# Kernel optimization log

Measured on AMD Instinct MI355X. Metric: run time of the kernel, lower is better.

The kernel has to match this reference:

```python
import jax, jax.numpy as jnp
import numpy as np

N = 50000      # nodes
E = 800000     # edges (before self-loops)
IN_DIM = 128
HID = 64
HEADS = 4
NEG_SLOPE = 0.2  # PyG GATConv default leaky-relu slope


def setup_inputs() -> dict:
    key = jax.random.key(0)
    ks = jax.random.split(key, 12)
    s = 0.05
    return {
        "x": jax.random.normal(ks[0], (N, IN_DIM), jnp.float32),
        "edge_index": jax.random.randint(ks[1], (2, E), 0, N, dtype=jnp.int64),
        "W1": jax.random.normal(ks[2], (IN_DIM, HEADS * HID), jnp.float32) * s,
        "att1_src": jax.random.normal(ks[3], (HEADS, HID), jnp.float32) * s,
        "att1_dst": jax.random.normal(ks[4], (HEADS, HID), jnp.float32) * s,
        "b1": jax.random.normal(ks[5], (HEADS * HID,), jnp.float32) * s,
        "W2": jax.random.normal(ks[6], (HEADS * HID, HID), jnp.float32) * s,
        "att2_src": jax.random.normal(ks[7], (1, HID), jnp.float32) * s,
        "att2_dst": jax.random.normal(ks[8], (1, HID), jnp.float32) * s,
        "b2": jax.random.normal(ks[9], (HID,), jnp.float32) * s,
        "Wc": jax.random.normal(ks[10], (HID, 2), jnp.float32) * s,
        "bc": jax.random.normal(ks[11], (2,), jnp.float32) * s,
    }


def _gat_conv(x, src, dst, W, a_src, a_dst, b, heads, d, concat):
    """PyG GATConv (eval mode): gather-score-segment_softmax-scatter."""
    n = x.shape[0]
    h = (x @ W).reshape(n, heads, d)               # [N,H,D]
    alpha_s = jnp.einsum('nhd,hd->nh', h, a_src)   # [N,H]
    alpha_d = jnp.einsum('nhd,hd->nh', h, a_dst)
    e = jax.nn.leaky_relu(alpha_s[src] + alpha_d[dst], NEG_SLOPE)  # [E,H]
    # softmax over incoming edges of each destination node
    m = jax.ops.segment_max(e, dst, num_segments=n)                # [N,H]
    ex = jnp.exp(e - m[dst])
    den = jax.ops.segment_sum(ex, dst, num_segments=n)
    alpha = ex / den[dst]                                          # [E,H]
    out = jax.ops.segment_sum(h[src] * alpha[:, :, None], dst, num_segments=n)  # [N,H,D]
    out = out.reshape(n, heads * d) if concat else out.mean(axis=1)
    return out + b


def reference(x, edge_index, W1, att1_src, att1_dst, b1,
              W2, att2_src, att2_dst, b2, Wc, bc):
    n = x.shape[0]
    # PyG GATConv adds self-loops by default
    loops = jnp.arange(n, dtype=edge_index.dtype)
    src = jnp.concatenate([edge_index[0], loops])
    dst = jnp.concatenate([edge_index[1], loops])
    h1 = jax.nn.elu(_gat_conv(x, src, dst, W1, att1_src, att1_dst, b1, HEADS, HID, True))
    h2 = jax.nn.elu(_gat_conv(h1, src, dst, W2, att2_src, att2_dst, b2, 1, HID, False))
    return h2 @ Wc + bc
```

## Files before the change

kernel.cpp:

```cpp
#include <hip/hip_runtime.h>
#include <hip/hip_bf16.h>
#include <cstddef>


#define HEADS 4
#define HID 64
#define IN_DIM 128

using bf16x8 = __attribute__((ext_vector_type(8))) short;
using f32x4  = __attribute__((ext_vector_type(4))) float;

__device__ __forceinline__ float us2f(unsigned short u) {
    return __uint_as_float((unsigned int)u << 16);
}
__device__ __forceinline__ unsigned short f2us(float f) {
    __hip_bfloat16 b = __float2bfloat16(f);
    return __builtin_bit_cast(unsigned short, b);
}

__global__ __launch_bounds__(256) void cvt_w_kernel(const float* __restrict__ W,
                                                    unsigned short* __restrict__ WT,
                                                    int K, int Ncol) {
    int i = blockIdx.x * 256 + threadIdx.x;
    if (i >= K * Ncol) return;
    int k = i / Ncol, n = i - k * Ncol;
    WT[(size_t)n * K + k] = f2us(W[i]);
}

template <int BN, int BK, int KFULL, bool INTERLEAVE, bool AF32>
__global__ __launch_bounds__(256) void gemm_mfma_kernel(
    const void* __restrict__ Av,
    const unsigned short* __restrict__ BT,
    unsigned short* __restrict__ C,
    int M, int Nfull) {
    constexpr int LDK = BK + 8;
    constexpr int NT = BN / 16;
    constexpr int KC = BK / 8;
    __shared__ unsigned short As[64 * LDK];
    __shared__ unsigned short Bs[BN * LDK];
    const int tid = threadIdx.x;
    const int wave = tid >> 6, lane = tid & 63;
    const int row0 = blockIdx.y * 64;
    const int col0 = blockIdx.x * BN;
    f32x4 acc[NT] = {};
    for (int k0 = 0; k0 < KFULL; k0 += BK) {
        for (int c = tid; c < 64 * KC; c += 256) {
            int r = c / KC, kc = c - r * KC;
            int row = row0 + r; if (row >= M) row = M - 1;
            if constexpr (AF32) {
                const float* Af = (const float*)Av;
                const float* src = Af + (size_t)row * KFULL + k0 + kc * 8;
                float4 v0 = *(const float4*)(src);
                float4 v1 = *(const float4*)(src + 4);
                ushort4 lo = make_ushort4(f2us(v0.x), f2us(v0.y), f2us(v0.z), f2us(v0.w));
                ushort4 hi = make_ushort4(f2us(v1.x), f2us(v1.y), f2us(v1.z), f2us(v1.w));
                *(ushort4*)(As + r * LDK + kc * 8) = lo;
                *(ushort4*)(As + r * LDK + kc * 8 + 4) = hi;
            } else {
                const unsigned short* Ab = (const unsigned short*)Av;
                *(bf16x8*)(As + r * LDK + kc * 8) =
                    *(const bf16x8*)(Ab + (size_t)row * KFULL + k0 + kc * 8);
            }
        }
        for (int c = tid; c < BN * KC; c += 256) {
            int r = c / KC, kc = c - r * KC;
            *(bf16x8*)(Bs + r * LDK + kc * 8) =
                *(const bf16x8*)(BT + (size_t)(col0 + r) * KFULL + k0 + kc * 8);
        }
        __syncthreads();
        const int arow = wave * 16 + (lane & 15);
        const int kb = (lane >> 4) * 8;
#pragma unroll
        for (int ks = 0; ks < BK; ks += 32) {
            bf16x8 af = *(const bf16x8*)(As + arow * LDK + ks + kb);
#pragma unroll
            for (int nt = 0; nt < NT; ++nt) {
                bf16x8 bfv = *(const bf16x8*)(Bs + (nt * 16 + (lane & 15)) * LDK + ks + kb);
                acc[nt] = __builtin_amdgcn_mfma_f32_16x16x32_bf16(af, bfv, acc[nt], 0, 0, 0);
            }
        }
        __syncthreads();
    }
    const int crow0 = row0 + wave * 16 + ((lane >> 4) << 2);
#pragma unroll
    for (int nt = 0; nt < NT; ++nt) {
        const int col = col0 + nt * 16 + (lane & 15);
#pragma unroll
        for (int j = 0; j < 4; ++j) {
            const int row = crow0 + j;
            if (row < M) {
                size_t off = INTERLEAVE
                    ? (size_t)row * 256 + (size_t)(col & 63) * 4 + (col >> 6)
                    : (size_t)row * Nfull + col;
                C[off] = f2us(acc[nt][j]);
            }
        }
    }
}

__global__ void deg_init_kernel(int* __restrict__ deg, int N) {
    int n = blockIdx.x * 256 + threadIdx.x;
    if (n < N) deg[n] = 1;
}
__global__ void deg_count_kernel(const int* __restrict__ dst, int* __restrict__ deg, int E) {
    int e = blockIdx.x * 256 + threadIdx.x;
    if (e < E) atomicAdd(&deg[dst[e]], 1);
}
__global__ __launch_bounds__(256) void scan1_kernel(const int* __restrict__ deg,
                                                    int* __restrict__ bsum, int N) {
    const int i = blockIdx.x * 256 + threadIdx.x;
    const int lane = threadIdx.x & 63, w = threadIdx.x >> 6;
    int v = (i < N) ? deg[i] : 0;
#pragma unroll
    for (int off = 32; off; off >>= 1) v += __shfl_xor(v, off, 64);
    __shared__ int ws[4];
    if (lane == 0) ws[w] = v;
    __syncthreads();
    if (threadIdx.x == 0) bsum[blockIdx.x] = ws[0] + ws[1] + ws[2] + ws[3];
}
__global__ __launch_bounds__(256) void scan2_kernel(const int* __restrict__ bsum,
                                                    int* __restrict__ boff, int nb) {
    const int tid = threadIdx.x, lane = tid & 63, w = tid >> 6;
    int v = (tid < nb) ? bsum[tid] : 0;
    int x = v;
#pragma unroll
    for (int off = 1; off < 64; off <<= 1) {
        int y = __shfl_up(x, off, 64);
        if (lane >= off) x += y;
    }
    __shared__ int ws[4];
    if (lane == 63) ws[w] = x;
    __syncthreads();
    int add = 0;
    for (int i = 0; i < w; ++i) add += ws[i];
    x += add;
    if (tid < nb) boff[tid] = x - v;
    if (tid == 255) boff[nb] = x;
}
__global__ __launch_bounds__(256) void scan3_kernel(const int* __restrict__ deg,
                                                    const int* __restrict__ boff,
                                                    int* __restrict__ row_ptr, int N) {
    const int i = blockIdx.x * 256 + threadIdx.x;
    const int tid = threadIdx.x, lane = tid & 63, w = tid >> 6;
    int v = (i < N) ? deg[i] : 0;
    int x = v;
#pragma unroll
    for (int off = 1; off < 64; off <<= 1) {
        int y = __shfl_up(x, off, 64);
        if (lane >= off) x += y;
    }
    __shared__ int ws[4];
    if (lane == 63) ws[w] = x;
    __syncthreads();
    int add = 0;
    for (int k = 0; k < w; ++k) add += ws[k];
    x += add;
    int excl = x - v + boff[blockIdx.x];
    if (i < N) row_ptr[i] = excl;
    if (i == N - 1) row_ptr[N] = excl + v;
}
__global__ void selfloop_kernel(const int* __restrict__ row_ptr, int* __restrict__ colA,
                                int* __restrict__ dstA, int* __restrict__ fill, int N) {
    int n = blockIdx.x * 256 + threadIdx.x;
    if (n < N) {
        int p = row_ptr[n];
        colA[p] = n;
        dstA[p] = n;
        fill[n] = p + 1;
    }
}
__global__ void scatter_kernel(const int* __restrict__ src, const int* __restrict__ dst,
                               int* __restrict__ fill, int* __restrict__ colA,
                               int* __restrict__ dstA, int E) {
    int e = blockIdx.x * 256 + threadIdx.x;
    if (e < E) {
        int d = dst[e];
        int pos = atomicAdd(&fill[d], 1);
        colA[pos] = src[e];
        dstA[pos] = d;
    }
}

__global__ __launch_bounds__(256) void alpha1_kernel(const unsigned short* __restrict__ g1,
                                                     const float* __restrict__ a_src,
                                                     const float* __restrict__ a_dst,
                                                     float* __restrict__ as1,
                                                     float* __restrict__ ad1, int N) {
    int wid = (blockIdx.x * 256 + threadIdx.x) >> 6;
    int lane = threadIdx.x & 63;
    if (wid >= N) return;
    ushort4 g = *(const ushort4*)(g1 + (size_t)wid * 256 + lane * 4);
    float f0 = us2f(g.x), f1 = us2f(g.y), f2 = us2f(g.z), f3 = us2f(g.w);
    float s0 = f0 * a_src[lane],       d0 = f0 * a_dst[lane];
    float s1 = f1 * a_src[64 + lane],  d1 = f1 * a_dst[64 + lane];
    float s2 = f2 * a_src[128 + lane], d2 = f2 * a_dst[128 + lane];
    float s3 = f3 * a_src[192 + lane], d3 = f3 * a_dst[192 + lane];
#pragma unroll
    for (int off = 32; off; off >>= 1) {
        s0 += __shfl_xor(s0, off, 64); d0 += __shfl_xor(d0, off, 64);
        s1 += __shfl_xor(s1, off, 64); d1 += __shfl_xor(d1, off, 64);
        s2 += __shfl_xor(s2, off, 64); d2 += __shfl_xor(d2, off, 64);
        s3 += __shfl_xor(s3, off, 64); d3 += __shfl_xor(d3, off, 64);
    }
    if (lane == 0) {
        *(float4*)(as1 + (size_t)wid * 4) = make_float4(s0, s1, s2, s3);
        *(float4*)(ad1 + (size_t)wid * 4) = make_float4(d0, d1, d2, d3);
    }
}
__global__ __launch_bounds__(256) void alpha2_kernel(const unsigned short* __restrict__ g2,
                                                     const float* __restrict__ a_src,
                                                     const float* __restrict__ a_dst,
                                                     float* __restrict__ as2,
                                                     float* __restrict__ ad2, int N) {
    int wid = (blockIdx.x * 256 + threadIdx.x) >> 6;
    int lane = threadIdx.x & 63;
    if (wid >= N) return;
    float v = us2f(g2[(size_t)wid * 64 + lane]);
    float s = v * a_src[lane];
    float d = v * a_dst[lane];
#pragma unroll
    for (int off = 32; off; off >>= 1) {
        s += __shfl_xor(s, off, 64);
        d += __shfl_xor(d, off, 64);
    }
    if (lane == 0) { as2[wid] = s; ad2[wid] = d; }
}

template <int H>
__global__ __launch_bounds__(256) void wkernel(const int* __restrict__ colA,
                                               const int* __restrict__ dstA,
                                               const float* __restrict__ as,
                                               const float* __restrict__ ad,
                                               float* __restrict__ wA, int NNZ) {
    int p = blockIdx.x * 256 + threadIdx.x;
    if (p >= NNZ) return;
    const int src = colA[p], dst = dstA[p];
    if constexpr (H == 4) {
        float4 s = *(const float4*)(as + (size_t)src * 4);
        float4 d = *(const float4*)(ad + (size_t)dst * 4);
        float e;
        float4 w;
        e = s.x + d.x; e = e > 0.f ? e : 0.2f * e; w.x = __expf(e);
        e = s.y + d.y; e = e > 0.f ? e : 0.2f * e; w.y = __expf(e);
        e = s.z + d.z; e = e > 0.f ? e : 0.2f * e; w.z = __expf(e);
        e = s.w + d.w; e = e > 0.f ? e : 0.2f * e; w.w = __expf(e);
        *(float4*)(wA + (size_t)p * 4) = w;
    } else {
        float e = as[src] + ad[dst];
        e = e > 0.f ? e : 0.2f * e;
        wA[p] = __expf(e);
    }
}

__global__ __launch_bounds__(256) void agg1_kernel(
    const unsigned short* __restrict__ g1, const float* __restrict__ wA,
    const int* __restrict__ row_ptr, const int* __restrict__ colA,
    const float* __restrict__ b1, unsigned short* __restrict__ h1b, int N) {
    int wid = (blockIdx.x * 256 + threadIdx.x) >> 6;
    int lane = threadIdx.x & 63;
    if (wid >= N) return;
    float s0 = 0.f, s1 = 0.f, s2 = 0.f, s3 = 0.f;
    float a0 = 0.f, a1 = 0.f, a2 = 0.f, a3 = 0.f;
    const int beg = row_ptr[wid], end = row_ptr[wid + 1];
    for (int idx = beg; idx < end; idx += 8) {
        int p[8];
#pragma unroll
        for (int j = 0; j < 8; ++j) { int q = idx + j; p[j] = q < end ? q : end - 1; }
        int si[8];
#pragma unroll
        for (int j = 0; j < 8; ++j) si[j] = colA[p[j]];
        float4 w[8];
#pragma unroll
        for (int j = 0; j < 8; ++j) w[j] = *(const float4*)(wA + (size_t)p[j] * 4);
        ushort4 g[8];
#pragma unroll
        for (int j = 0; j < 8; ++j)
            g[j] = *(const ushort4*)(g1 + ((size_t)si[j] << 8) + lane * 4);
#pragma unroll
        for (int j = 0; j < 8; ++j) {
            const float m = (idx + j < end) ? 1.f : 0.f;
            const float wx = w[j].x * m, wy = w[j].y * m;
            const float wz = w[j].z * m, ww = w[j].w * m;
            s0 += wx; a0 += wx * us2f(g[j].x);
            s1 += wy; a1 += wy * us2f(g[j].y);
            s2 += wz; a2 += wz * us2f(g[j].z);
            s3 += ww; a3 += ww * us2f(g[j].w);
        }
    }
    size_t base = (size_t)wid * 256;
    float o;
    o = a0 / s0 + b1[lane];       o = o > 0.f ? o : expm1f(o); h1b[base + lane]       = f2us(o);
    o = a1 / s1 + b1[64 + lane];  o = o > 0.f ? o : expm1f(o); h1b[base + 64 + lane]  = f2us(o);
    o = a2 / s2 + b1[128 + lane]; o = o > 0.f ? o : expm1f(o); h1b[base + 128 + lane] = f2us(o);
    o = a3 / s3 + b1[192 + lane]; o = o > 0.f ? o : expm1f(o); h1b[base + 192 + lane] = f2us(o);
}

__global__ __launch_bounds__(256) void agg2_kernel(
    const unsigned short* __restrict__ g2, const float* __restrict__ wA,
    const int* __restrict__ row_ptr, const int* __restrict__ colA,
    const float* __restrict__ b2, const float* __restrict__ Wc,
    const float* __restrict__ bc, float* __restrict__ out, int N) {
    int wid = (blockIdx.x * 256 + threadIdx.x) >> 6;
    int lane = threadIdx.x & 63;
    if (wid >= N) return;
    float s = 0.f, a = 0.f;
    const int beg = row_ptr[wid], end = row_ptr[wid + 1];
    for (int idx = beg; idx < end; idx += 16) {
        int p[16];
#pragma unroll
        for (int j = 0; j < 16; ++j) { int q = idx + j; p[j] = q < end ? q : end - 1; }
        int si[16];
#pragma unroll
        for (int j = 0; j < 16; ++j) si[j] = colA[p[j]];
        float w[16];
#pragma unroll
        for (int j = 0; j < 16; ++j) w[j] = wA[p[j]];
        unsigned short g[16];
#pragma unroll
        for (int j = 0; j < 16; ++j) g[j] = g2[((size_t)si[j] << 6) + lane];
#pragma unroll
        for (int j = 0; j < 16; ++j) {
            const float m = (idx + j < end) ? 1.f : 0.f;
            const float wj = w[j] * m;
            s += wj; a += wj * us2f(g[j]);
        }
    }
    float h = a / s + b2[lane];
    h = h > 0.f ? h : expm1f(h);
    float c0 = h * Wc[lane * 2 + 0];
    float c1 = h * Wc[lane * 2 + 1];
#pragma unroll
    for (int off = 32; off; off >>= 1) {
        c0 += __shfl_xor(c0, off, 64);
        c1 += __shfl_xor(c1, off, 64);
    }
    if (lane == 0) {
        out[(size_t)wid * 2 + 0] = c0 + bc[0];
        out[(size_t)wid * 2 + 1] = c1 + bc[1];
    }
}

extern "C" void kernel_launch(void* const* d_in, const int* in_sizes, int n_in,
                              void* d_out, int out_size, void* d_ws, size_t ws_size,
                              hipStream_t stream) {
    const float* x        = (const float*)d_in[0];
    const int*   ei       = (const int*)d_in[1];
    const float* W1       = (const float*)d_in[2];
    const float* att1_src = (const float*)d_in[3];
    const float* att1_dst = (const float*)d_in[4];
    const float* b1       = (const float*)d_in[5];
    const float* W2       = (const float*)d_in[6];
    const float* att2_src = (const float*)d_in[7];
    const float* att2_dst = (const float*)d_in[8];
    const float* b2       = (const float*)d_in[9];
    const float* Wc       = (const float*)d_in[10];
    const float* bc       = (const float*)d_in[11];
    float* out = (float*)d_out;

    const int N = in_sizes[0] / IN_DIM;
    const int E = in_sizes[1] / 2;
    const int NNZ = E + N;
    const int* srcI = ei;
    const int* dstI = ei + E;

    unsigned short* g1b = (unsigned short*)d_ws;
    unsigned short* h1b = g1b + (size_t)N * 256;
    unsigned short* g2b = h1b + (size_t)N * 256;
    unsigned short* W1T = g2b + (size_t)N * 64;
    unsigned short* W2T = W1T + 256 * 128;
    float* as1 = (float*)(W2T + 64 * 256);
    float* ad1 = as1 + (size_t)N * 4;
    float* as2 = ad1 + (size_t)N * 4;
    float* ad2 = as2 + N;
    float* wA1 = ad2 + N;
    float* wA2 = wA1 + (size_t)NNZ * 4;
    int* deg     = (int*)(wA2 + NNZ);
    int* row_ptr = deg + N;
    int* fill    = row_ptr + N + 1;
    int* bsum    = fill + N;
    int* boff    = bsum + 256;
    int* colA    = boff + 260;
    int* dstA    = colA + NNZ;

    const int nB = (N + 255) / 256;
    const int eB = (E + 255) / 256;
    const int pB = (NNZ + 255) / 256;
    const int wB = ((N * 64) + 255) / 256;
    const int nb = nB;

    cvt_w_kernel<<<(IN_DIM * 256 + 255) / 256, 256, 0, stream>>>(W1, W1T, IN_DIM, 256);
    cvt_w_kernel<<<(256 * 64 + 255) / 256, 256, 0, stream>>>(W2, W2T, 256, 64);

    deg_init_kernel<<<nB, 256, 0, stream>>>(deg, N);
    deg_count_kernel<<<eB, 256, 0, stream>>>(dstI, deg, E);
    scan1_kernel<<<nB, 256, 0, stream>>>(deg, bsum, N);
    scan2_kernel<<<1, 256, 0, stream>>>(bsum, boff, nb);
    scan3_kernel<<<nB, 256, 0, stream>>>(deg, boff, row_ptr, N);
    selfloop_kernel<<<nB, 256, 0, stream>>>(row_ptr, colA, dstA, fill, N);
    scatter_kernel<<<eB, 256, 0, stream>>>(srcI, dstI, fill, colA, dstA, E);

    gemm_mfma_kernel<128, 128, 128, true, true>
        <<<dim3(2, (N + 63) / 64), 256, 0, stream>>>(x, W1T, g1b, N, 256);
    alpha1_kernel<<<wB, 256, 0, stream>>>(g1b, att1_src, att1_dst, as1, ad1, N);
    wkernel<4><<<pB, 256, 0, stream>>>(colA, dstA, as1, ad1, wA1, NNZ);
    agg1_kernel<<<wB, 256, 0, stream>>>(g1b, wA1, row_ptr, colA, b1, h1b, N);

    gemm_mfma_kernel<64, 128, 256, false, false>
        <<<dim3(1, (N + 63) / 64), 256, 0, stream>>>(h1b, W2T, g2b, N, 64);
    alpha2_kernel<<<wB, 256, 0, stream>>>(g2b, att2_src, att2_dst, as2, ad2, N);
    wkernel<1><<<pB, 256, 0, stream>>>(colA, dstA, as2, ad2, wA2, NNZ);
    agg2_kernel<<<wB, 256, 0, stream>>>(g2b, wA2, row_ptr, colA, b2, Wc, bc, out, N);
}
```

Baseline: 410.3 us.

## Split each node's aggregation across two waves and fuse setup kernels

The agg1 and agg2 kernels now give each destination node two wavefronts, which take alternating chunks of edges and combine their partial sums through shared memory before the epilogue. The aim is more memory-level parallelism for the gather-bound aggregation, at the cost of twice as many waves, a block-wide barrier and extra shared memory. Separately, the two weight-conversion kernels and the degree-init kernel are merged into one launch to cut launch overhead.

```diff
diff --git a/kernel.cpp b/kernel.cpp
--- a/kernel.cpp
+++ b/kernel.cpp
@@ -18,13 +18,21 @@
     return __builtin_bit_cast(unsigned short, b);
 }
 
-__global__ __launch_bounds__(256) void cvt_w_kernel(const float* __restrict__ W,
-                                                    unsigned short* __restrict__ WT,
-                                                    int K, int Ncol) {
+__global__ __launch_bounds__(256) void setup_kernel(const float* __restrict__ W1,
+                                                    const float* __restrict__ W2,
+                                                    unsigned short* __restrict__ W1T,
+                                                    unsigned short* __restrict__ W2T,
+                                                    int* __restrict__ deg, int N) {
     int i = blockIdx.x * 256 + threadIdx.x;
-    if (i >= K * Ncol) return;
-    int k = i / Ncol, n = i - k * Ncol;
-    WT[(size_t)n * K + k] = f2us(W[i]);
+    if (i < N) deg[i] = 1;
+    if (i < IN_DIM * 256) {
+        int k = i >> 8, n = i & 255;
+        W1T[n * IN_DIM + k] = f2us(W1[i]);
+    }
+    if (i < 256 * 64) {
+        int k = i >> 6, n = i & 63;
+        W2T[n * 256 + k] = f2us(W2[i]);
+    }
 }
 
 template <int BN, int BK, int KFULL, bool INTERLEAVE, bool AF32>
@@ -48,18 +56,16 @@
             int r = c / KC, kc = c - r * KC;
             int row = row0 + r; if (row >= M) row = M - 1;
             if constexpr (AF32) {
-                const float* Af = (const float*)Av;
-                const float* src = Af + (size_t)row * KFULL + k0 + kc * 8;
+                const float* src = (const float*)Av + (size_t)row * KFULL + k0 + kc * 8;
                 float4 v0 = *(const float4*)(src);
                 float4 v1 = *(const float4*)(src + 4);
-                ushort4 lo = make_ushort4(f2us(v0.x), f2us(v0.y), f2us(v0.z), f2us(v0.w));
-                ushort4 hi = make_ushort4(f2us(v1.x), f2us(v1.y), f2us(v1.z), f2us(v1.w));
-                *(ushort4*)(As + r * LDK + kc * 8) = lo;
-                *(ushort4*)(As + r * LDK + kc * 8 + 4) = hi;
+                *(ushort4*)(As + r * LDK + kc * 8) =
+                    make_ushort4(f2us(v0.x), f2us(v0.y), f2us(v0.z), f2us(v0.w));
+                *(ushort4*)(As + r * LDK + kc * 8 + 4) =
+                    make_ushort4(f2us(v1.x), f2us(v1.y), f2us(v1.z), f2us(v1.w));
             } else {
-                const unsigned short* Ab = (const unsigned short*)Av;
                 *(bf16x8*)(As + r * LDK + kc * 8) =
-                    *(const bf16x8*)(Ab + (size_t)row * KFULL + k0 + kc * 8);
+                    *(const bf16x8*)((const unsigned short*)Av + (size_t)row * KFULL + k0 + kc * 8);
             }
         }
         for (int c = tid; c < BN * KC; c += 256) {
@@ -98,10 +104,6 @@
     }
 }
 
-__global__ void deg_init_kernel(int* __restrict__ deg, int N) {
-    int n = blockIdx.x * 256 + threadIdx.x;
-    if (n < N) deg[n] = 1;
-}
 __global__ void deg_count_kernel(const int* __restrict__ dst, int* __restrict__ deg, int E) {
     int e = blockIdx.x * 256 + threadIdx.x;
     if (e < E) atomicAdd(&deg[dst[e]], 1);
@@ -256,43 +258,59 @@
     const unsigned short* __restrict__ g1, const float* __restrict__ wA,
     const int* __restrict__ row_ptr, const int* __restrict__ colA,
     const float* __restrict__ b1, unsigned short* __restrict__ h1b, int N) {
-    int wid = (blockIdx.x * 256 + threadIdx.x) >> 6;
-    int lane = threadIdx.x & 63;
-    if (wid >= N) return;
+    const int gw = (blockIdx.x * 256 + threadIdx.x) >> 6;
+    const int node = gw >> 1, sub = gw & 1;
+    const int lane = threadIdx.x & 63, lw = threadIdx.x >> 6;
+    __shared__ float sh_a[4][64][4];
+    __shared__ float sh_s[4][4];
     float s0 = 0.f, s1 = 0.f, s2 = 0.f, s3 = 0.f;
     float a0 = 0.f, a1 = 0.f, a2 = 0.f, a3 = 0.f;
-    const int beg = row_ptr[wid], end = row_ptr[wid + 1];
-    for (int idx = beg; idx < end; idx += 8) {
-        int p[8];
-#pragma unroll
-        for (int j = 0; j < 8; ++j) { int q = idx + j; p[j] = q < end ? q : end - 1; }
-        int si[8];
-#pragma unroll
-        for (int j = 0; j < 8; ++j) si[j] = colA[p[j]];
-        float4 w[8];
-#pragma unroll
-        for (int j = 0; j < 8; ++j) w[j] = *(const float4*)(wA + (size_t)p[j] * 4);
-        ushort4 g[8];
-#pragma unroll
-        for (int j = 0; j < 8; ++j)
-            g[j] = *(const ushort4*)(g1 + ((size_t)si[j] << 8) + lane * 4);
-#pragma unroll
-        for (int j = 0; j < 8; ++j) {
-            const float m = (idx + j < end) ? 1.f : 0.f;
-            const float wx = w[j].x * m, wy = w[j].y * m;
-            const float wz = w[j].z * m, ww = w[j].w * m;
-            s0 += wx; a0 += wx * us2f(g[j].x);
-            s1 += wy; a1 += wy * us2f(g[j].y);
-            s2 += wz; a2 += wz * us2f(g[j].z);
-            s3 += ww; a3 += ww * us2f(g[j].w);
-        }
-    }
-    size_t base = (size_t)wid * 256;
-    float o;
-    o = a0 / s0 + b1[lane];       o = o > 0.f ? o : expm1f(o); h1b[base + lane]       = f2us(o);
-    o = a1 / s1 + b1[64 + lane];  o = o > 0.f ? o : expm1f(o); h1b[base + 64 + lane]  = f2us(o);
-    o = a2 / s2 + b1[128 + lane]; o = o > 0.f ? o : expm1f(o); h1b[base + 128 + lane] = f2us(o);
-    o = a3 / s3 + b1[192 + lane]; o = o > 0.f ? o : expm1f(o); h1b[base + 192 + lane] = f2us(o);
+    if (node < N) {
+        const int beg = row_ptr[node], end = row_ptr[node + 1];
+        for (int idx = beg + sub * 8; idx < end; idx += 16) {
+            int p[8];
+#pragma unroll
+            for (int j = 0; j < 8; ++j) { int q = idx + j; p[j] = q < end ? q : end - 1; }
+            int si[8];
+#pragma unroll
+            for (int j = 0; j < 8; ++j) si[j] = colA[p[j]];
+            float4 w[8];
+#pragma unroll
+            for (int j = 0; j < 8; ++j) w[j] = *(const float4*)(wA + (size_t)p[j] * 4);
+            ushort4 g[8];
+#pragma unroll
+            for (int j = 0; j < 8; ++j)
+                g[j] = *(const ushort4*)(g1 + ((size_t)si[j] << 8) + lane * 4);
+#pragma unroll
+            for (int j = 0; j < 8; ++j) {
+                const float m = (idx + j < end) ? 1.f : 0.f;
+                const float wx = w[j].x * m, wy = w[j].y * m;
+                const float wz = w[j].z * m, ww = w[j].w * m;
+                s0 += wx; a0 += wx * us2f(g[j].x);
+                s1 += wy; a1 += wy * us2f(g[j].y);
+                s2 += wz; a2 += wz * us2f(g[j].z);
+                s3 += ww; a3 += ww * us2f(g[j].w);
+            }
+        }
+    }
+    sh_a[lw][lane][0] = a0; sh_a[lw][lane][1] = a1;
+    sh_a[lw][lane][2] = a2; sh_a[lw][lane][3] = a3;
+    if (lane == 0) {
+        sh_s[lw][0] = s0; sh_s[lw][1] = s1; sh_s[lw][2] = s2; sh_s[lw][3] = s3;
+    }
+    __syncthreads();
+    if (sub == 0 && node < N) {
+        a0 += sh_a[lw + 1][lane][0]; a1 += sh_a[lw + 1][lane][1];
+        a2 += sh_a[lw + 1][lane][2]; a3 += sh_a[lw + 1][lane][3];
+        s0 += sh_s[lw + 1][0]; s1 += sh_s[lw + 1][1];
+        s2 += sh_s[lw + 1][2]; s3 += sh_s[lw + 1][3];
+        size_t base = (size_t)node * 256;
+        float o;
+        o = a0 / s0 + b1[lane];       o = o > 0.f ? o : expm1f(o); h1b[base + lane]       = f2us(o);
+        o = a1 / s1 + b1[64 + lane];  o = o > 0.f ? o : expm1f(o); h1b[base + 64 + lane]  = f2us(o);
+        o = a2 / s2 + b1[128 + lane]; o = o > 0.f ? o : expm1f(o); h1b[base + 128 + lane] = f2us(o);
+        o = a3 / s3 + b1[192 + lane]; o = o > 0.f ? o : expm1f(o); h1b[base + 192 + lane] = f2us(o);
+    }
 }
 
 __global__ __launch_bounds__(256) void agg2_kernel(
@@ -300,43 +318,54 @@
     const int* __restrict__ row_ptr, const int* __restrict__ colA,
     const float* __restrict__ b2, const float* __restrict__ Wc,
     const float* __restrict__ bc, float* __restrict__ out, int N) {
-    int wid = (blockIdx.x * 256 + threadIdx.x) >> 6;
-    int lane = threadIdx.x & 63;
-    if (wid >= N) return;
+    const int gw = (blockIdx.x * 256 + threadIdx.x) >> 6;
+    const int node = gw >> 1, sub = gw & 1;
+    const int lane = threadIdx.x & 63, lw = threadIdx.x >> 6;
+    __shared__ float sh_a[4][64];
+    __shared__ float sh_s[4];
     float s = 0.f, a = 0.f;
-    const int beg = row_ptr[wid], end = row_ptr[wid + 1];
-    for (int idx = beg; idx < end; idx += 16) {
-        int p[16];
-#pragma unroll
-        for (int j = 0; j < 16; ++j) { int q = idx + j; p[j] = q < end ? q : end - 1; }
-        int si[16];
-#pragma unroll
-        for (int j = 0; j < 16; ++j) si[j] = colA[p[j]];
-        float w[16];
-#pragma unroll
-        for (int j = 0; j < 16; ++j) w[j] = wA[p[j]];
-        unsigned short g[16];
-#pragma unroll
-        for (int j = 0; j < 16; ++j) g[j] = g2[((size_t)si[j] << 6) + lane];
-#pragma unroll
-        for (int j = 0; j < 16; ++j) {
-            const float m = (idx + j < end) ? 1.f : 0.f;
-            const float wj = w[j] * m;
-            s += wj; a += wj * us2f(g[j]);
-        }
-    }
-    float h = a / s + b2[lane];
-    h = h > 0.f ? h : expm1f(h);
-    float c0 = h * Wc[lane * 2 + 0];
-    float c1 = h * Wc[lane * 2 + 1];
-#pragma unroll
-    for (int off = 32; off; off >>= 1) {
-        c0 += __shfl_xor(c0, off, 64);
-        c1 += __shfl_xor(c1, off, 64);
-    }
-    if (lane == 0) {
-        out[(size_t)wid * 2 + 0] = c0 + bc[0];
-        out[(size_t)wid * 2 + 1] = c1 + bc[1];
+    if (node < N) {
+        const int beg = row_ptr[node], end = row_ptr[node + 1];
+        for (int idx = beg + sub * 16; idx < end; idx += 32) {
+            int p[16];
+#pragma unroll
+            for (int j = 0; j < 16; ++j) { int q = idx + j; p[j] = q < end ? q : end - 1; }
+            int si[16];
+#pragma unroll
+            for (int j = 0; j < 16; ++j) si[j] = colA[p[j]];
+            float w[16];
+#pragma unroll
+            for (int j = 0; j < 16; ++j) w[j] = wA[p[j]];
+            unsigned short g[16];
+#pragma unroll
+            for (int j = 0; j < 16; ++j) g[j] = g2[((size_t)si[j] << 6) + lane];
+#pragma unroll
+            for (int j = 0; j < 16; ++j) {
+                const float m = (idx + j < end) ? 1.f : 0.f;
+                const float wj = w[j] * m;
+                s += wj; a += wj * us2f(g[j]);
+            }
+        }
+    }
+    sh_a[lw][lane] = a;
+    if (lane == 0) sh_s[lw] = s;
+    __syncthreads();
+    if (sub == 0 && node < N) {
+        a += sh_a[lw + 1][lane];
+        s += sh_s[lw + 1];
+        float h = a / s + b2[lane];
+        h = h > 0.f ? h : expm1f(h);
+        float c0 = h * Wc[lane * 2 + 0];
+        float c1 = h * Wc[lane * 2 + 1];
+#pragma unroll
+        for (int off = 32; off; off >>= 1) {
+            c0 += __shfl_xor(c0, off, 64);
+            c1 += __shfl_xor(c1, off, 64);
+        }
+        if (lane == 0) {
+            out[(size_t)node * 2 + 0] = c0 + bc[0];
+            out[(size_t)node * 2 + 1] = c1 + bc[1];
+        }
     }
 }
 
@@ -386,12 +415,11 @@
     const int eB = (E + 255) / 256;
     const int pB = (NNZ + 255) / 256;
     const int wB = ((N * 64) + 255) / 256;
+    const int w2B = ((N * 128) + 255) / 256;
     const int nb = nB;
 
-    cvt_w_kernel<<<(IN_DIM * 256 + 255) / 256, 256, 0, stream>>>(W1, W1T, IN_DIM, 256);
-    cvt_w_kernel<<<(256 * 64 + 255) / 256, 256, 0, stream>>>(W2, W2T, 256, 64);
-
-    deg_init_kernel<<<nB, 256, 0, stream>>>(deg, N);
+    setup_kernel<<<nB, 256, 0, stream>>>(W1, W2, W1T, W2T, deg, N);
+
     deg_count_kernel<<<eB, 256, 0, stream>>>(dstI, deg, E);
     scan1_kernel<<<nB, 256, 0, stream>>>(deg, bsum, N);
     scan2_kernel<<<1, 256, 0, stream>>>(bsum, boff, nb);
@@ -403,11 +431,11 @@
         <<<dim3(2, (N + 63) / 64), 256, 0, stream>>>(x, W1T, g1b, N, 256);
     alpha1_kernel<<<wB, 256, 0, stream>>>(g1b, att1_src, att1_dst, as1, ad1, N);
     wkernel<4><<<pB, 256, 0, stream>>>(colA, dstA, as1, ad1, wA1, NNZ);
-    agg1_kernel<<<wB, 256, 0, stream>>>(g1b, wA1, row_ptr, colA, b1, h1b, N);
+    agg1_kernel<<<w2B, 256, 0, stream>>>(g1b, wA1, row_ptr, colA, b1, h1b, N);
 
     gemm_mfma_kernel<64, 128, 256, false, false>
         <<<dim3(1, (N + 63) / 64), 256, 0, stream>>>(h1b, W2T, g2b, N, 64);
     alpha2_kernel<<<wB, 256, 0, stream>>>(g2b, att2_src, att2_dst, as2, ad2, N);
     wkernel<1><<<pB, 256, 0, stream>>>(colA, dstA, as2, ad2, wA2, NNZ);
-    agg2_kernel<<<wB, 256, 0, stream>>>(g2b, wA2, row_ptr, colA, b2, Wc, bc, out, N);
-}
+    agg2_kernel<<<w2B, 256, 0, stream>>>(g2b, wA2, row_ptr, colA, b2, Wc, bc, out, N);
+}
```

New measurement: 454.4 us. 10.8% more time.
